# Performance work log

Measured on AMD Instinct MI355X. Metric: run time of the kernel, lower is better.

Reference implementation:

```python
import math
import jax, jax.numpy as jnp
import numpy as np

B, N, CS, CZ, CH, H, PQ, PV = 1, 4096, 512, 128, 64, 16, 4, 8
BQ, BK = 32, 128
NB = N // BQ
CZ4 = CZ // 4
INF = 100000.0
EPS = 1e-8


def quat_to_rot(q):
    w, x, y, z = q[..., 0], q[..., 1], q[..., 2], q[..., 3]
    return jnp.stack([
        jnp.stack([1 - 2 * (y * y + z * z), 2 * (x * y - w * z), 2 * (x * z + w * y)], -1),
        jnp.stack([2 * (x * y + w * z), 1 - 2 * (x * x + z * z), 2 * (y * z - w * x)], -1),
        jnp.stack([2 * (x * z - w * y), 2 * (y * z + w * x), 1 - 2 * (x * x + y * y)], -1),
    ], -2)


def setup_inputs() -> dict:
    key = jax.random.key(0)
    ks = jax.random.split(key, 16)
    s = jax.random.normal(ks[0], (B, N, CS), jnp.float32)
    z = jax.random.normal(ks[1], (B, NB, BQ, BK, CZ), jnp.float32)
    trans = jax.random.normal(ks[2], (B, N, 3), jnp.float32) * 10.0
    quat = jax.random.normal(ks[3], (B, N, 4), jnp.float32)
    quat = quat / jnp.linalg.norm(quat, axis=-1, keepdims=True)
    rots = quat_to_rot(quat)
    s_mask = jnp.ones((B, N), jnp.float32)
    pad = (BK - BQ) // 2  # key window centered on each query block
    key_idx = (jnp.arange(NB)[:, None] * BQ - pad + jnp.arange(BK)[None, :]).astype(jnp.int32)

    def w(k, shp):
        return jax.random.normal(k, shp, jnp.float32) * (1.0 / math.sqrt(shp[0]))

    return {
        's': s, 'z': z, 'trans': trans, 'rots': rots, 's_mask': s_mask, 'key_idx': key_idx,
        'Wq': w(ks[4], (CS, H * CH)), 'Wk': w(ks[5], (CS, H * CH)), 'Wv': w(ks[6], (CS, H * CH)),
        'Wqp': w(ks[7], (CS, H * PQ * 3)), 'Wkvp': w(ks[8], (CS, H * (PQ + PV) * 3)),
        'Wb': w(ks[9], (CZ, H)), 'Wdz': w(ks[10], (CZ, CZ4)),
        'head_weights': jnp.full((H,), float(np.log(np.e - 1.0)), jnp.float32),  # softplus^-1(1)
        'Wout': w(ks[11], (H * (CZ4 + CH + PV * 4), CS)),
        'g_s': jnp.ones((CS,), jnp.float32), 'b_s': jnp.zeros((CS,), jnp.float32),
        'g_z': jnp.ones((CZ,), jnp.float32), 'b_z': jnp.zeros((CZ,), jnp.float32),
    }


def _ln(x, g, b):
    m = jnp.mean(x, -1, keepdims=True)
    v = jnp.mean((x - m) ** 2, -1, keepdims=True)
    return (x - m) * jax.lax.rsqrt(v + 1e-5) * g + b


def _ipa(s, z, trans, rots, s_mask, key_idx, Wq, Wk, Wv, Wqp, Wkvp, Wb, Wdz,
         head_weights, Wout, g_s, b_s, g_z, b_z):
    s_n = _ln(s, g_s, b_s)
    z_n = _ln(z, g_z, b_z)

    valid = (key_idx >= 0) & (key_idx < N)            # [NB, BK]
    idx = jnp.clip(key_idx, 0, N - 1)
    vf = valid.astype(s.dtype)[None]                  # [1, NB, BK]

    def gk(x):  # gather key window: [B,N,...] -> [B,NB,BK,...]
        return x[:, idx]

    sq = s_n.reshape(B, NB, BQ, CS)
    sk = gk(s_n) * vf[..., None]                      # zero-pad out-of-range keys

    tq = trans.reshape(B, NB, BQ, 3)
    rq = rots.reshape(B, NB, BQ, 3, 3)
    tk = gk(trans) * vf[..., None]
    rk = jnp.where(valid[None, :, :, None, None], gk(rots), jnp.eye(3, dtype=rots.dtype))

    q = (sq @ Wq).reshape(B, NB, BQ, H, CH)
    k = (sk @ Wk).reshape(B, NB, BK, H, CH)
    v = (sk @ Wv).reshape(B, NB, BK, H, CH)

    q_pts = (sq @ Wqp).reshape(B, NB, BQ, H * PQ, 3)
    q_pts = jnp.einsum('bnqij,bnqpj->bnqpi', rq, q_pts) + tq[:, :, :, None, :]
    q_pts = q_pts.reshape(B, NB, BQ, H, PQ, 3)

    kv_pts = (sk @ Wkvp).reshape(B, NB, BK, H * (PQ + PV), 3)
    kv_pts = jnp.einsum('bnkij,bnkpj->bnkpi', rk, kv_pts) + tk[:, :, :, None, :]
    kv_pts = kv_pts.reshape(B, NB, BK, H, PQ + PV, 3)
    k_pts, v_pts = kv_pts[..., :PQ, :], kv_pts[..., PQ:, :]

    bias = jnp.einsum('bnqkc,ch->bnqkh', z_n, Wb)
    a = jnp.einsum('bnqhc,bnkhc->bnqkh', q, k) * math.sqrt(1.0 / (3 * CH))
    a = a + math.sqrt(1.0 / 3) * bias

    disp = q_pts[:, :, :, None] - k_pts[:, :, None]   # [B,NB,BQ,BK,H,PQ,3]
    pt_att = jnp.sum(disp ** 2, -1)                   # [B,NB,BQ,BK,H,PQ]
    hw = jax.nn.softplus(head_weights) * math.sqrt(1.0 / (3 * (PQ * 9.0 / 2)))
    pt_att = -0.5 * jnp.sum(pt_att * hw[:, None], -1)  # [B,NB,BQ,BK,H]

    qm = s_mask.reshape(B, NB, BQ)
    km = gk(s_mask) * vf
    amask = INF * (qm[:, :, :, None] * km[:, :, None, :] - 1.0)

    a = a + pt_att + amask[..., None]
    a = jax.nn.softmax(jnp.swapaxes(a, -1, -2), axis=-1)  # [B,NB,BQ,H,BK]

    o = jnp.einsum('bnqhk,bnkhc->bnqhc', a, v).reshape(B, NB, BQ, H * CH)

    o_pt = jnp.einsum('bnqhk,bnkhpc->bnqhpc', a, v_pts)
    o_pt = jnp.einsum('bnqji,bnqhpj->bnqhpi', rq, o_pt - tq[:, :, :, None, None, :])
    o_pt_norm = jnp.sqrt(jnp.sum(o_pt ** 2, -1) + EPS).reshape(B, NB, BQ, H * PV)
    o_pt = o_pt.reshape(B, NB, BQ, H * PV * 3)

    pair_z = z_n @ Wdz                                # [B,NB,BQ,BK,CZ4]
    o_pair = jnp.einsum('bnqhk,bnqkc->bnqhc', a, pair_z).reshape(B, NB, BQ, H * CZ4)

    out = jnp.concatenate([o, o_pt, o_pt_norm, o_pair], -1) @ Wout
    return out.reshape(B, N, CS)


def reference(s, z, trans, rots, s_mask, key_idx, Wq, Wk, Wv, Wqp, Wkvp, Wb, Wdz,
              head_weights, Wout, g_s, b_s, g_z, b_z):
    return _ipa(s, z, trans, rots, s_mask, key_idx, Wq, Wk, Wv, Wqp, Wkvp, Wb, Wdz,
                head_weights, Wout, g_s, b_s, g_z, b_z)
```

## Files before the change

### kernel.cpp

```cpp
#include <hip/hip_runtime.h>
#include <math.h>

#define D_N 4096
#define PBW 3072
#define PPW 768
#define OFFK 1024
#define OFFV 2048
#define CATW 2048

typedef __bf16 bf16_t;
typedef __bf16 bf16x8 __attribute__((ext_vector_type(8)));
typedef __bf16 bf16x4 __attribute__((ext_vector_type(4)));
typedef float f32x4 __attribute__((ext_vector_type(4)));

__device__ __forceinline__ void gld16(const void* g, void* l) {
    __builtin_amdgcn_global_load_lds((const __attribute__((address_space(1))) unsigned int*)g,
                                     (__attribute__((address_space(3))) unsigned int*)l, 16, 0, 0);
}

__global__ __launch_bounds__(256) void k_prep(
    const float* __restrict__ Wq, const float* __restrict__ Wk, const float* __restrict__ Wv,
    const float* __restrict__ Wqp, const float* __restrict__ Wkvp, const float* __restrict__ Wout,
    const float* __restrict__ Wb, const float* __restrict__ Wdz,
    const float* __restrict__ gz, const float* __restrict__ bz,
    const float* __restrict__ s, const float* __restrict__ g_s, const float* __restrict__ b_s,
    bf16_t* __restrict__ wcatT, bf16_t* __restrict__ WoutT,
    bf16_t* __restrict__ WzT, float* __restrict__ Kv, bf16_t* __restrict__ s_nb)
{
    __shared__ float T[64][65];
    const int bx = blockIdx.x;
    const int tid = threadIdx.x;
    if (bx < 736) {
        const float* src; int ld, coff, r0;
        bf16_t* dst; int Rdst;
        if (bx < 480) {
            int c0 = (bx % 60) * 64;
            r0 = (bx / 60) * 64;
            if (c0 < 1024)      { src = Wq;   ld = 1024; coff = c0; }
            else if (c0 < 2048) { src = Wk;   ld = 1024; coff = c0 - 1024; }
            else if (c0 < 3072) { src = Wv;   ld = 1024; coff = c0 - 2048; }
            else if (c0 < 3264) { src = Wqp;  ld = 192;  coff = c0 - 3072; }
            else                { src = Wkvp; ld = 576;  coff = c0 - 3264; }
            dst = wcatT + (size_t)c0 * 512; Rdst = 512;
        } else {
            int b = bx - 480;
            int c0 = (b & 7) * 64;
            r0 = (b >> 3) * 64;
            src = Wout; ld = 512; coff = c0;
            dst = WoutT + (size_t)c0 * 2048; Rdst = 2048;
        }
        {
            int rr = tid >> 2, cb = (tid & 3) * 16;
            const float* p = src + (size_t)(r0 + rr) * ld + coff + cb;
            #pragma unroll
            for (int i = 0; i < 4; ++i)
                *(float4*)&T[rr][cb + i * 4] = *(const float4*)(p + i * 4);
        }
        __syncthreads();
        {
            int cc = tid >> 2, rb = (tid & 3) * 16;
            bf16_t* o = dst + (size_t)cc * Rdst + r0 + rb;
            bf16x8 o0, o1;
            #pragma unroll
            for (int j = 0; j < 8; ++j) o0[j] = (bf16_t)T[rb + j][cc];
            #pragma unroll
            for (int j = 0; j < 8; ++j) o1[j] = (bf16_t)T[rb + 8 + j][cc];
            *(bf16x8*)(o) = o0;
            *(bf16x8*)(o + 8) = o1;
        }
    } else if (bx == 736) {
        for (int i = tid; i < 6144; i += 256) {
            int j = i >> 7, c = i & 127;
            float w = (j < 16) ? Wb[c * 16 + j] : Wdz[c * 32 + (j - 16)];
            WzT[i] = (bf16_t)(gz[c] * w);
        }
        if (tid < 48) {
            int j = tid;
            float acc = 0.f;
            for (int c = 0; c < 128; ++c) {
                float w = (j < 16) ? Wb[c * 16 + j] : Wdz[c * 32 + (j - 16)];
                acc += bz[c] * w;
            }
            Kv[j] = acc;
        }
    } else {
        int row = (bx - 737) * 4 + (tid >> 6);
        int lane = tid & 63;
        const float4* p = (const float4*)(s + (size_t)row * 512);
        float4 v0 = p[lane];
        float4 v1 = p[lane + 64];
        float sum = v0.x + v0.y + v0.z + v0.w + v1.x + v1.y + v1.z + v1.w;
        float sq  = v0.x*v0.x + v0.y*v0.y + v0.z*v0.z + v0.w*v0.w
                  + v1.x*v1.x + v1.y*v1.y + v1.z*v1.z + v1.w*v1.w;
        #pragma unroll
        for (int off = 1; off < 64; off <<= 1) {
            sum += __shfl_xor(sum, off);
            sq  += __shfl_xor(sq, off);
        }
        float m = sum * (1.0f / 512.0f);
        float var = sq * (1.0f / 512.0f) - m * m;
        float rs = rsqrtf(var + 1e-5f);
        int c = lane * 4;
        int c2 = 256 + lane * 4;
        bf16x4 r0, r1;
        r0[0] = (bf16_t)((v0.x - m) * rs * g_s[c+0] + b_s[c+0]);
        r0[1] = (bf16_t)((v0.y - m) * rs * g_s[c+1] + b_s[c+1]);
        r0[2] = (bf16_t)((v0.z - m) * rs * g_s[c+2] + b_s[c+2]);
        r0[3] = (bf16_t)((v0.w - m) * rs * g_s[c+3] + b_s[c+3]);
        r1[0] = (bf16_t)((v1.x - m) * rs * g_s[c2+0] + b_s[c2+0]);
        r1[1] = (bf16_t)((v1.y - m) * rs * g_s[c2+1] + b_s[c2+1]);
        r1[2] = (bf16_t)((v1.z - m) * rs * g_s[c2+2] + b_s[c2+2]);
        r1[3] = (bf16_t)((v1.w - m) * rs * g_s[c2+3] + b_s[c2+3]);
        *(bf16x4*)(s_nb + (size_t)row * 512 + c)  = r0;
        *(bf16x4*)(s_nb + (size_t)row * 512 + c2) = r1;
    }
}

__global__ __launch_bounds__(256) void k_fused(
    const bf16_t* __restrict__ A, const bf16_t* __restrict__ BT,
    bf16_t* __restrict__ projb, float* __restrict__ projp,
    const float* __restrict__ z, const bf16_t* __restrict__ WzT, const float* __restrict__ Kv,
    bf16_t* __restrict__ biasT, bf16_t* __restrict__ pzT)
{
    __shared__ bf16_t Asl[128][32];
    __shared__ bf16_t Bsl[128][32];
    const int bx = blockIdx.x;
    const int tid = threadIdx.x, lane = tid & 63, w = tid >> 6;
    int gemm_id = -1, zid = 0;
    if (bx < 2880) {
        int s3 = bx % 3, b3 = bx / 3;
        if (s3 == 0) gemm_id = b3;
        else         zid = b3 * 2 + s3 - 1;
    } else {
        zid = 1920 + (bx - 2880);
    }

    if (gemm_id >= 0) {
        const int row0 = (gemm_id / 30) * 128, col0 = (gemm_id % 30) * 128;
        const int wr = (w >> 1) * 64, wc = (w & 1) * 64;
        const int K = 512;
        const int sr = lane >> 2, k8 = (lane & 3) * 8;
        const bf16_t* Ab = A + (size_t)(row0 + w * 32 + sr) * K + k8;
        const bf16_t* Bb = BT + (size_t)(col0 + w * 32 + sr) * K + k8;
        f32x4 acc[4][4];
        #pragma unroll
        for (int m = 0; m < 4; ++m)
            #pragma unroll
            for (int n = 0; n < 4; ++n) acc[m][n] = (f32x4){0.f,0.f,0.f,0.f};
        for (int k0 = 0; k0 < K; k0 += 32) {
            __syncthreads();
            gld16(Ab + k0,          &Asl[w * 32][0]);
            gld16(Ab + k0 + 16 * K, &Asl[w * 32 + 16][0]);
            gld16(Bb + k0,          &Bsl[w * 32][0]);
            gld16(Bb + k0 + 16 * K, &Bsl[w * 32 + 16][0]);
            __syncthreads();
            bf16x8 af[4], bfr[4];
            #pragma unroll
            for (int m = 0; m < 4; ++m) af[m]  = *(const bf16x8*)&Asl[wr + m*16 + (lane & 15)][(lane >> 4) * 8];
            #pragma unroll
            for (int n = 0; n < 4; ++n) bfr[n] = *(const bf16x8*)&Bsl[wc + n*16 + (lane & 15)][(lane >> 4) * 8];
            #pragma unroll
            for (int m = 0; m < 4; ++m)
                #pragma unroll
                for (int n = 0; n < 4; ++n)
                    acc[m][n] = __builtin_amdgcn_mfma_f32_16x16x32_bf16(af[m], bfr[n], acc[m][n], 0, 0, 0);
        }
        if (col0 < 3072) {
            #pragma unroll
            for (int m = 0; m < 4; ++m)
                #pragma unroll
                for (int n = 0; n < 4; ++n)
                    #pragma unroll
                    for (int i = 0; i < 4; ++i)
                        projb[(size_t)(row0 + wr + m*16 + (lane >> 4)*4 + i) * PBW + col0 + wc + n*16 + (lane & 15)]
                            = (bf16_t)acc[m][n][i];
        } else {
            #pragma unroll
            for (int m = 0; m < 4; ++m)
                #pragma unroll
                for (int n = 0; n < 4; ++n)
                    #pragma unroll
                    for (int i = 0; i < 4; ++i)
                        projp[(size_t)(row0 + wr + m*16 + (lane >> 4)*4 + i) * PPW + col0 - 3072 + wc + n*16 + (lane & 15)]
                            = acc[m][n][i];
        }
        return;
    }

    const int r16 = lane & 15, kg = lane >> 4;
    bf16x8 bfz[3][4];
    #pragma unroll
    for (int nt = 0; nt < 3; ++nt)
        #pragma unroll
        for (int kc = 0; kc < 4; ++kc)
            bfz[nt][kc] = *(const bf16x8*)(WzT + (size_t)(nt * 16 + r16) * 128 + kc * 32 + kg * 8);
    const float K0 = Kv[r16], K1 = Kv[16 + r16], K2 = Kv[32 + r16];
    const int gid = zid * 4 + w;

    #pragma unroll 2
    for (int it = 0; it < 4; ++it) {
        const int t_ = gid * 4 + it;
        const float* zp = z + ((size_t)t_ * 16 + r16) * 128 + kg * 8;
        float4 za[4], zc[4];
        float sum = 0.f, sq = 0.f;
        #pragma unroll
        for (int kc = 0; kc < 4; ++kc) {
            za[kc] = *(const float4*)(zp + kc * 32);
            zc[kc] = *(const float4*)(zp + kc * 32 + 4);
            sum += za[kc].x + za[kc].y + za[kc].z + za[kc].w + zc[kc].x + zc[kc].y + zc[kc].z + zc[kc].w;
            sq  += za[kc].x*za[kc].x + za[kc].y*za[kc].y + za[kc].z*za[kc].z + za[kc].w*za[kc].w
                 + zc[kc].x*zc[kc].x + zc[kc].y*zc[kc].y + zc[kc].z*zc[kc].z + zc[kc].w*zc[kc].w;
        }
        sum += __shfl_xor(sum, 16); sq += __shfl_xor(sq, 16);
        sum += __shfl_xor(sum, 32); sq += __shfl_xor(sq, 32);
        float m_ = sum * (1.0f / 128.0f);
        float rs_ = rsqrtf(sq * (1.0f / 128.0f) - m_ * m_ + 1e-5f);
        bf16x8 af[4];
        #pragma unroll
        for (int kc = 0; kc < 4; ++kc) {
            af[kc][0] = (bf16_t)((za[kc].x - m_) * rs_);
            af[kc][1] = (bf16_t)((za[kc].y - m_) * rs_);
            af[kc][2] = (bf16_t)((za[kc].z - m_) * rs_);
            af[kc][3] = (bf16_t)((za[kc].w - m_) * rs_);
            af[kc][4] = (bf16_t)((zc[kc].x - m_) * rs_);
            af[kc][5] = (bf16_t)((zc[kc].y - m_) * rs_);
            af[kc][6] = (bf16_t)((zc[kc].z - m_) * rs_);
            af[kc][7] = (bf16_t)((zc[kc].w - m_) * rs_);
        }
        f32x4 acc0 = (f32x4){0.f,0.f,0.f,0.f};
        f32x4 acc1 = (f32x4){0.f,0.f,0.f,0.f};
        f32x4 acc2 = (f32x4){0.f,0.f,0.f,0.f};
        #pragma unroll
        for (int kc = 0; kc < 4; ++kc) {
            acc0 = __builtin_amdgcn_mfma_f32_16x16x32_bf16(af[kc], bfz[0][kc], acc0, 0, 0, 0);
            acc1 = __builtin_amdgcn_mfma_f32_16x16x32_bf16(af[kc], bfz[1][kc], acc1, 0, 0, 0);
            acc2 = __builtin_amdgcn_mfma_f32_16x16x32_bf16(af[kc], bfz[2][kc], acc2, 0, 0, 0);
        }
        const int rowq_ = t_ >> 3;
        const int k0_ = ((t_ & 7) << 4) + kg * 4;
        bf16x4 bb, p1, p2;
        #pragma unroll
        for (int i2 = 0; i2 < 4; ++i2) {
            bb[i2] = (bf16_t)(acc0[i2] + K0);
            p1[i2] = (bf16_t)(acc1[i2] + K1);
            p2[i2] = (bf16_t)(acc2[i2] + K2);
        }
        *(bf16x4*)&biasT[((size_t)rowq_ * 16 + r16) * 128 + k0_] = bb;
        *(bf16x4*)&pzT[((size_t)rowq_ * 32 + r16) * 128 + k0_] = p1;
        *(bf16x4*)&pzT[((size_t)rowq_ * 32 + 16 + r16) * 128 + k0_] = p2;
    }
}

__global__ __launch_bounds__(256, 3) void k_attn4(
    const bf16_t* __restrict__ projb, const float* __restrict__ projp,
    const bf16_t* __restrict__ biasT, const float* __restrict__ rots,
    const float* __restrict__ trans, const float* __restrict__ smask,
    const int* __restrict__ kidx, const float* __restrict__ hwraw,
    bf16_t* __restrict__ catb, bf16_t* __restrict__ Pbf)
{
    __shared__ __align__(16) char pool[51840];
    bf16_t (*Qs)[72]   = (bf16_t(*)[72])pool;
    bf16_t (*Ks)[72]   = (bf16_t(*)[72])(pool + 32 * 72 * 2);
    bf16_t (*Vt)[136]  = (bf16_t(*)[136])pool;
    float  (*att)[132] = (float(*)[132])(pool + 26112);
    bf16_t (*Ps)[136]  = (bf16_t(*)[136])(pool + 26112);
    float  (*optmp)[33]= (float(*)[33])(pool + 26112 + 8704);
    float  (*kp_s)[12] = (float(*)[12])(pool + 43008);
    float  (*qp_s)[12] = (float(*)[12])(pool + 49152);
    float*  km_s       = (float*)(pool + 50688);
    float*  qm_s       = (float*)(pool + 51200);

    const int wgid = blockIdx.x;
    const int swz = (wgid & 7) * 256 + (wgid >> 3);
    const int h = swz >> 7;
    const int nblk = swz & 127;
    const int tid = threadIdx.x;
    const int lane = tid & 63;
    const int w = tid >> 6;
    const int rowq0 = nblk * 32;
    const float hw = log1pf(__expf(hwraw[h])) * 0.13608276348795434f;

    const int kslot = tid & 127;
    const int ki = kidx[nblk * 128 + kslot];
    const int kvalid = (ki >= 0 && ki < D_N);
    const int myrow = ki < 0 ? 0 : (ki > D_N - 1 ? D_N - 1 : ki);

    {
        int q = tid >> 3, cg = (tid & 7) * 8;
        *(bf16x8*)&Qs[q][cg] = *(const bf16x8*)(projb + (size_t)(rowq0 + q) * PBW + h * 64 + cg);
    }
    float Rk[9], tk0 = 0.f, tk1 = 0.f, tk2 = 0.f;
    bf16x8 vreg[8];
    if (tid < 128) {
        km_s[tid] = kvalid ? smask[myrow] : 0.0f;
        const float* Rp = rots + (size_t)myrow * 9;
        const float* tp = trans + (size_t)myrow * 3;
        #pragma unroll
        for (int e = 0; e < 9; ++e) Rk[e] = Rp[e];
        tk0 = tp[0]; tk1 = tp[1]; tk2 = tp[2];
        const float* kp = projp + (size_t)myrow * PPW + 192 + h * 36;
        float4 p0 = *(const float4*)kp;
        float4 p1 = *(const float4*)(kp + 4);
        float4 p2 = *(const float4*)(kp + 8);
        float xs[4] = {p0.x, p0.w, p1.z, p2.y};
        float ys[4] = {p0.y, p1.x, p1.w, p2.z};
        float zs[4] = {p0.z, p1.y, p2.x, p2.w};
        #pragma unroll
        for (int p = 0; p < 4; ++p) {
            kp_s[tid][p*3+0] = Rk[0]*xs[p] + Rk[1]*ys[p] + Rk[2]*zs[p] + tk0;
            kp_s[tid][p*3+1] = Rk[3]*xs[p] + Rk[4]*ys[p] + Rk[5]*zs[p] + tk1;
            kp_s[tid][p*3+2] = Rk[6]*xs[p] + Rk[7]*ys[p] + Rk[8]*zs[p] + tk2;
        }
    } else {
        if (tid < 160) qm_s[tid - 128] = smask[rowq0 + tid - 128];
        int j = tid - 128;
        {
            int q = j >> 2, p = j & 3;
            const float* Rp = rots + (size_t)(rowq0 + q) * 9;
            const float* tp = trans + (size_t)(rowq0 + q) * 3;
            const float* qp = projp + (size_t)(rowq0 + q) * PPW + h * 12 + p * 3;
            float x = qp[0], y = qp[1], zc = qp[2];
            qp_s[q][p*3+0] = Rp[0]*x + Rp[1]*y + Rp[2]*zc + tp[0];
            qp_s[q][p*3+1] = Rp[3]*x + Rp[4]*y + Rp[5]*zc + tp[1];
            qp_s[q][p*3+2] = Rp[6]*x + Rp[7]*y + Rp[8]*zc + tp[2];
        }
        {
            const bf16_t* pK = projb + (size_t)myrow * PBW + OFFK + h * 64;
            #pragma unroll
            for (int u = 0; u < 8; ++u)
                *(bf16x8*)&Ks[j][u * 8] = *(const bf16x8*)(pK + u * 8);
        }
        {
            const bf16_t* pV = projb + (size_t)myrow * PBW + OFFV + h * 64;
            #pragma unroll
            for (int u4 = 0; u4 < 8; ++u4)
                vreg[u4] = *(const bf16x8*)(pV + u4 * 8);
        }
    }
    float bT_reg[16];
    {
        int q = tid >> 3, kg = tid & 7;
        const bf16_t* bT = biasT + ((size_t)(rowq0 + q) * 16 + h) * 128 + kg;
        #pragma unroll
        for (int j2 = 0; j2 < 16; ++j2) bT_reg[j2] = (float)bT[j2 * 8];
    }
    __syncthreads();
    {
        #pragma unroll
        for (int j = 0; j < 4; ++j) {
            int T = w * 4 + j;
            int m = T & 1, n = T >> 1;
            f32x4 acc = (f32x4){0.f,0.f,0.f,0.f};
            #pragma unroll
            for (int kc = 0; kc < 2; ++kc) {
                bf16x8 a = *(const bf16x8*)&Qs[m*16 + (lane & 15)][kc*32 + (lane >> 4) * 8];
                bf16x8 b = *(const bf16x8*)&Ks[n*16 + (lane & 15)][kc*32 + (lane >> 4) * 8];
                acc = __builtin_amdgcn_mfma_f32_16x16x32_bf16(a, b, acc, 0, 0, 0);
            }
            #pragma unroll
            for (int i = 0; i < 4; ++i)
                att[m*16 + (lane >> 4)*4 + i][n*16 + (lane & 15)] = acc[i];
        }
    }
    __syncthreads();
    if (tid < 128) {
        const float* vp = projp + (size_t)myrow * PPW + 192 + h * 36 + 12;
        float4 a0 = *(const float4*)(vp);
        float4 a1 = *(const float4*)(vp + 4);
        float4 a2 = *(const float4*)(vp + 8);
        float4 a3 = *(const float4*)(vp + 12);
        float4 a4 = *(const float4*)(vp + 16);
        float4 a5 = *(const float4*)(vp + 20);
        float xs[8] = {a0.x, a0.w, a1.z, a2.y, a3.x, a3.w, a4.z, a5.y};
        float ys[8] = {a0.y, a1.x, a1.w, a2.z, a3.y, a4.x, a4.w, a5.z};
        float zs[8] = {a0.z, a1.y, a2.x, a2.w, a3.z, a4.y, a5.x, a5.w};
        #pragma unroll
        for (int p = 0; p < 8; ++p) {
            Vt[64 + p*3 + 0][tid] = (bf16_t)(Rk[0]*xs[p] + Rk[1]*ys[p] + Rk[2]*zs[p] + tk0);
            Vt[64 + p*3 + 1][tid] = (bf16_t)(Rk[3]*xs[p] + Rk[4]*ys[p] + Rk[5]*zs[p] + tk1);
            Vt[64 + p*3 + 2][tid] = (bf16_t)(Rk[6]*xs[p] + Rk[7]*ys[p] + Rk[8]*zs[p] + tk2);
        }
        {
            bf16x8 zz = {};
            *(bf16x8*)&Vt[88 + (tid & 7)][(tid >> 3) * 8] = zz;
        }
    } else {
        int krow = tid - 128;
        #pragma unroll
        for (int u4 = 0; u4 < 8; ++u4) {
            #pragma unroll
            for (int jj = 0; jj < 8; ++jj) Vt[u4 * 8 + jj][krow] = vreg[u4][jj];
        }
    }
    {
        int q = tid >> 3, kg = tid & 7;
        float qp[12];
        #pragma unroll
        for (int e = 0; e < 12; ++e) qp[e] = qp_s[q][e];
        float qm = qm_s[q];
        #pragma unroll
        for (int j2 = 0; j2 < 16; ++j2) {
            int k = kg + j2 * 8;
            float4 k0 = *(const float4*)&kp_s[k][0];
            float4 k1 = *(const float4*)&kp_s[k][4];
            float4 k2 = *(const float4*)&kp_s[k][8];
            float d0 = qp[0]-k0.x, d1 = qp[1]-k0.y, d2_ = qp[2]-k0.z, d3 = qp[3]-k0.w;
            float d4 = qp[4]-k1.x, d5 = qp[5]-k1.y, d6 = qp[6]-k1.z, d7 = qp[7]-k1.w;
            float d8 = qp[8]-k2.x, d9 = qp[9]-k2.y, d10 = qp[10]-k2.z, d11 = qp[11]-k2.w;
            float dd = d0*d0+d1*d1+d2_*d2_+d3*d3+d4*d4+d5*d5+d6*d6+d7*d7+d8*d8+d9*d9+d10*d10+d11*d11;
            float val = att[q][k] * 0.07216878364870323f
                      + 0.5773502691896258f * bT_reg[j2]
                      + 100000.0f * (qm * km_s[k] - 1.0f)
                      - 0.5f * hw * dd;
            att[q][k] = val;
        }
    }
    __syncthreads();
    {
        int q = tid >> 3, kg = tid & 7;
        float l[16];
        #pragma unroll
        for (int j2 = 0; j2 < 16; ++j2) l[j2] = att[q][kg * 16 + j2];
        float mx = l[0];
        #pragma unroll
        for (int j2 = 1; j2 < 16; ++j2) mx = fmaxf(mx, l[j2]);
        mx = fmaxf(mx, __shfl_xor(mx, 1));
        mx = fmaxf(mx, __shfl_xor(mx, 2));
        mx = fmaxf(mx, __shfl_xor(mx, 4));
        float se = 0.f;
        #pragma unroll
        for (int j2 = 0; j2 < 16; ++j2) { l[j2] = __expf(l[j2] - mx); se += l[j2]; }
        se += __shfl_xor(se, 1);
        se += __shfl_xor(se, 2);
        se += __shfl_xor(se, 4);
        float inv = 1.0f / se;
        __syncthreads();
        bf16_t* pg = Pbf + ((size_t)(rowq0 + q) * 16 + h) * 128 + kg * 16;
        #pragma unroll
        for (int j4 = 0; j4 < 4; ++j4) {
            bf16x4 pb4;
            #pragma unroll
            for (int e = 0; e < 4; ++e) pb4[e] = (bf16_t)(l[j4 * 4 + e] * inv);
            *(bf16x4*)&Ps[q][kg * 16 + j4 * 4] = pb4;
            *(bf16x4*)(pg + j4 * 4) = pb4;
        }
    }
    __syncthreads();
    {
        #pragma unroll
        for (int j = 0; j < 3; ++j) {
            int T = w * 3 + j;
            int m = T & 1, n = T >> 1;
            f32x4 acc = (f32x4){0.f,0.f,0.f,0.f};
            #pragma unroll
            for (int kc = 0; kc < 4; ++kc) {
                bf16x8 a = *(const bf16x8*)&Ps[m*16 + (lane & 15)][kc*32 + (lane >> 4) * 8];
                bf16x8 b = *(const bf16x8*)&Vt[n*16 + (lane & 15)][kc*32 + (lane >> 4) * 8];
                acc = __builtin_amdgcn_mfma_f32_16x16x32_bf16(a, b, acc, 0, 0, 0);
            }
            int rowb = m * 16 + (lane >> 4) * 4;
            int col = lane & 15;
            if (n < 4) {
                #pragma unroll
                for (int i = 0; i < 4; ++i)
                    catb[(size_t)(rowq0 + rowb + i) * CATW + h * 64 + n * 16 + col] = (bf16_t)acc[i];
            } else {
                #pragma unroll
                for (int i = 0; i < 4; ++i)
                    optmp[rowb + i][(n - 4) * 16 + col] = acc[i];
            }
        }
    }
    __syncthreads();
    {
        int q = tid >> 3, pp = tid & 7;
        float sx = optmp[q][pp * 3 + 0];
        float sy = optmp[q][pp * 3 + 1];
        float sz = optmp[q][pp * 3 + 2];
        const float* R = rots + (size_t)(rowq0 + q) * 9;
        const float* t = trans + (size_t)(rowq0 + q) * 3;
        float x = sx - t[0], y = sy - t[1], z2 = sz - t[2];
        float ox = R[0] * x + R[3] * y + R[6] * z2;
        float oy = R[1] * x + R[4] * y + R[7] * z2;
        float oz = R[2] * x + R[5] * y + R[8] * z2;
        bf16_t* cp = catb + (size_t)(rowq0 + q) * CATW;
        cp[1024 + h * 24 + pp * 3 + 0] = (bf16_t)ox;
        cp[1024 + h * 24 + pp * 3 + 1] = (bf16_t)oy;
        cp[1024 + h * 24 + pp * 3 + 2] = (bf16_t)oz;
        cp[1408 + h * 8 + pp] = (bf16_t)sqrtf(ox * ox + oy * oy + oz * oz + 1e-8f);
    }
}

__global__ __launch_bounds__(256) void k_opair(const bf16_t* __restrict__ Pbf,
    const bf16_t* __restrict__ pzT, bf16_t* __restrict__ catb)
{
    int tid = threadIdx.x, lane = tid & 63, w = tid >> 6;
    size_t rowq = (size_t)blockIdx.x * 4 + w;
    const bf16_t* Pp = Pbf + rowq * 2048;
    const bf16_t* zp = pzT + rowq * 4096;
    bf16x8 pa[4];
    #pragma unroll
    for (int kc = 0; kc < 4; ++kc)
        pa[kc] = *(const bf16x8*)(Pp + (size_t)(lane & 15) * 128 + kc * 32 + (lane >> 4) * 8);
    #pragma unroll
    for (int ct = 0; ct < 2; ++ct) {
        f32x4 acc = (f32x4){0.f,0.f,0.f,0.f};
        #pragma unroll
        for (int kc = 0; kc < 4; ++kc) {
            bf16x8 b = *(const bf16x8*)(zp + (size_t)(ct * 16 + (lane & 15)) * 128 + kc * 32 + (lane >> 4) * 8);
            acc = __builtin_amdgcn_mfma_f32_16x16x32_bf16(pa[kc], b, acc, 0, 0, 0);
        }
        #pragma unroll
        for (int i = 0; i < 4; ++i) {
            int hh = (lane >> 4) * 4 + i;
            catb[rowq * CATW + 1536 + hh * 32 + ct * 16 + (lane & 15)] = (bf16_t)acc[i];
        }
    }
}

__global__ __launch_bounds__(256) void gemm_out(const bf16_t* __restrict__ A, const bf16_t* __restrict__ BT,
    float* __restrict__ C)
{
    __shared__ bf16_t Asl[64][32];
    __shared__ bf16_t Bsl[128][32];
    const int tid = threadIdx.x, lane = tid & 63, w = tid >> 6;
    const int by = blockIdx.x & 63, bxc = blockIdx.x >> 6;
    const int row0 = by * 64, col0 = bxc * 128;
    const int wr = (w >> 1) * 32, wc = (w & 1) * 64;
    const int K = 2048;
    const int sr = lane >> 2, k8 = (lane & 3) * 8;
    const bf16_t* Ab = A + (size_t)(row0 + w * 16 + sr) * K + k8;
    const bf16_t* Bb = BT + (size_t)(col0 + w * 32 + sr) * K + k8;
    f32x4 acc[2][4];
    #pragma unroll
    for (int m = 0; m < 2; ++m)
        #pragma unroll
        for (int n = 0; n < 4; ++n) acc[m][n] = (f32x4){0.f,0.f,0.f,0.f};
    for (int k0 = 0; k0 < K; k0 += 32) {
        __syncthreads();
        gld16(Ab + k0,          &Asl[w * 16][0]);
        gld16(Bb + k0,          &Bsl[w * 32][0]);
        gld16(Bb + k0 + 16 * K, &Bsl[w * 32 + 16][0]);
        __syncthreads();
        bf16x8 af[2], bfr[4];
        #pragma unroll
        for (int m = 0; m < 2; ++m) af[m]  = *(const bf16x8*)&Asl[wr + m*16 + (lane & 15)][(lane >> 4) * 8];
        #pragma unroll
        for (int n = 0; n < 4; ++n) bfr[n] = *(const bf16x8*)&Bsl[wc + n*16 + (lane & 15)][(lane >> 4) * 8];
        #pragma unroll
        for (int m = 0; m < 2; ++m)
            #pragma unroll
            for (int n = 0; n < 4; ++n)
                acc[m][n] = __builtin_amdgcn_mfma_f32_16x16x32_bf16(af[m], bfr[n], acc[m][n], 0, 0, 0);
    }
    #pragma unroll
    for (int m = 0; m < 2; ++m)
        #pragma unroll
        for (int n = 0; n < 4; ++n)
            #pragma unroll
            for (int i = 0; i < 4; ++i)
                C[(size_t)(row0 + wr + m*16 + (lane >> 4)*4 + i) * 512 + col0 + wc + n*16 + (lane & 15)] = acc[m][n][i];
}

extern "C" void kernel_launch(void* const* d_in, const int* in_sizes, int n_in,
                              void* d_out, int out_size, void* d_ws, size_t ws_size,
                              hipStream_t stream)
{
    (void)in_sizes; (void)n_in; (void)out_size;
    const float* s     = (const float*)d_in[0];
    const float* z     = (const float*)d_in[1];
    const float* trans = (const float*)d_in[2];
    const float* rots  = (const float*)d_in[3];
    const float* smask = (const float*)d_in[4];
    const int*   kidx  = (const int*)d_in[5];
    const float* Wq    = (const float*)d_in[6];
    const float* Wk    = (const float*)d_in[7];
    const float* Wv    = (const float*)d_in[8];
    const float* Wqp   = (const float*)d_in[9];
    const float* Wkvp  = (const float*)d_in[10];
    const float* Wb    = (const float*)d_in[11];
    const float* Wdz   = (const float*)d_in[12];
    const float* hw    = (const float*)d_in[13];
    const float* Wout  = (const float*)d_in[14];
    const float* g_s   = (const float*)d_in[15];
    const float* b_s   = (const float*)d_in[16];
    const float* g_z   = (const float*)d_in[17];
    const float* b_z   = (const float*)d_in[18];

    char* ws = (char*)d_ws;
    bf16_t* projb = (bf16_t*)(ws);
    float*  projp = (float*)(ws + 25165824);
    bf16_t* biasT = (bf16_t*)(ws + 37748736);
    bf16_t* wcatT = (bf16_t*)(ws + 71303168);
    bf16_t* s_nb  = (bf16_t*)(ws + 75235328);
    bf16_t* pzT   = (bf16_t*)(ws + 79429632);
    bf16_t* Pbf   = (bf16_t*)(ws + 112984064);
    bf16_t* catb  = (bf16_t*)(ws + 129761280);
    bf16_t* WoutT = (bf16_t*)(ws + 146538496);
    bf16_t* WzT   = (bf16_t*)(ws + 148635648);
    float*  Kv    = (float*)(ws + 148647936);
    if (ws_size < (size_t)148648128) return;
    float* out = (float*)d_out;

    k_prep<<<1761, 256, 0, stream>>>(Wq, Wk, Wv, Wqp, Wkvp, Wout, Wb, Wdz, g_z, b_z,
                                     s, g_s, b_s, wcatT, WoutT, WzT, Kv, s_nb);
    k_fused<<<3008, 256, 0, stream>>>(s_nb, wcatT, projb, projp, z, WzT, Kv, biasT, pzT);
    k_attn4<<<2048, 256, 0, stream>>>(projb, projp, biasT, rots, trans, smask, kidx, hw, catb, Pbf);
    k_opair<<<1024, 256, 0, stream>>>(Pbf, pzT, catb);
    gemm_out<<<256, 256, 0, stream>>>(catb, WoutT, out);
}
```

Measured before the change: 202.3 us.

## Fuse pair-output contraction into attention kernel and reswizzle block-to-XCD mapping

The separate k_opair kernel is removed. The attention-weighted pair-feature contraction now runs inside the attention kernel, reading the softmax probabilities straight from shared memory instead of writing them to a global Pbf buffer and reading them back. This saves a launch plus a write and read of the probability tensor, but pzT is read once per head block (16 times per query row) and the contraction runs as scalar FMAs instead of MFMA. The block index swizzle is also changed so that all heads of a query block land on the same XCD, to improve L2 reuse of pzT and projb.

Result: slower. 297.8 us (+47.2%).

```diff
diff --git a/kernel.cpp b/kernel.cpp
--- a/kernel.cpp
+++ b/kernel.cpp
@@ -251,12 +251,12 @@
     }
 }
 
-__global__ __launch_bounds__(256, 3) void k_attn4(
+__global__ __launch_bounds__(256, 3) void k_attn5(
     const bf16_t* __restrict__ projb, const float* __restrict__ projp,
     const bf16_t* __restrict__ biasT, const float* __restrict__ rots,
     const float* __restrict__ trans, const float* __restrict__ smask,
     const int* __restrict__ kidx, const float* __restrict__ hwraw,
-    bf16_t* __restrict__ catb, bf16_t* __restrict__ Pbf)
+    const bf16_t* __restrict__ pzT, bf16_t* __restrict__ catb)
 {
     __shared__ __align__(16) char pool[51840];
     bf16_t (*Qs)[72]   = (bf16_t(*)[72])pool;
@@ -271,9 +271,11 @@
     float*  qm_s       = (float*)(pool + 51200);
 
     const int wgid = blockIdx.x;
-    const int swz = (wgid & 7) * 256 + (wgid >> 3);
-    const int h = swz >> 7;
-    const int nblk = swz & 127;
+    const int xcd = wgid & 7;
+    const int lo2 = (wgid >> 3) & 3;
+    const int h   = (wgid >> 5) & 15;
+    const int hi  = wgid >> 9;
+    const int nblk = (hi << 5) | (xcd << 2) | lo2;
     const int tid = threadIdx.x;
     const int lane = tid & 63;
     const int w = tid >> 6;
@@ -435,14 +437,12 @@
         se += __shfl_xor(se, 4);
         float inv = 1.0f / se;
         __syncthreads();
-        bf16_t* pg = Pbf + ((size_t)(rowq0 + q) * 16 + h) * 128 + kg * 16;
         #pragma unroll
         for (int j4 = 0; j4 < 4; ++j4) {
             bf16x4 pb4;
             #pragma unroll
             for (int e = 0; e < 4; ++e) pb4[e] = (bf16_t)(l[j4 * 4 + e] * inv);
             *(bf16x4*)&Ps[q][kg * 16 + j4 * 4] = pb4;
-            *(bf16x4*)(pg + j4 * 4) = pb4;
         }
     }
     __syncthreads();
@@ -489,32 +489,27 @@
         cp[1024 + h * 24 + pp * 3 + 2] = (bf16_t)oz;
         cp[1408 + h * 8 + pp] = (bf16_t)sqrtf(ox * ox + oy * oy + oz * oz + 1e-8f);
     }
-}
-
-__global__ __launch_bounds__(256) void k_opair(const bf16_t* __restrict__ Pbf,
-    const bf16_t* __restrict__ pzT, bf16_t* __restrict__ catb)
-{
-    int tid = threadIdx.x, lane = tid & 63, w = tid >> 6;
-    size_t rowq = (size_t)blockIdx.x * 4 + w;
-    const bf16_t* Pp = Pbf + rowq * 2048;
-    const bf16_t* zp = pzT + rowq * 4096;
-    bf16x8 pa[4];
-    #pragma unroll
-    for (int kc = 0; kc < 4; ++kc)
-        pa[kc] = *(const bf16x8*)(Pp + (size_t)(lane & 15) * 128 + kc * 32 + (lane >> 4) * 8);
-    #pragma unroll
-    for (int ct = 0; ct < 2; ++ct) {
-        f32x4 acc = (f32x4){0.f,0.f,0.f,0.f};
-        #pragma unroll
-        for (int kc = 0; kc < 4; ++kc) {
-            bf16x8 b = *(const bf16x8*)(zp + (size_t)(ct * 16 + (lane & 15)) * 128 + kc * 32 + (lane >> 4) * 8);
-            acc = __builtin_amdgcn_mfma_f32_16x16x32_bf16(pa[kc], b, acc, 0, 0, 0);
-        }
-        #pragma unroll
-        for (int i = 0; i < 4; ++i) {
-            int hh = (lane >> 4) * 4 + i;
-            catb[rowq * CATW + 1536 + hh * 32 + ct * 16 + (lane & 15)] = (bf16_t)acc[i];
-        }
+    {
+        int q = tid >> 3, cg = (tid & 7) * 4;
+        const bf16_t* pzrow = pzT + ((size_t)(rowq0 + q) * 32 + cg) * 128;
+        float acc[4] = {0.f, 0.f, 0.f, 0.f};
+        #pragma unroll
+        for (int kc = 0; kc < 16; ++kc) {
+            bf16x8 ps8 = *(const bf16x8*)&Ps[q][kc * 8];
+            float psf[8];
+            #pragma unroll
+            for (int e = 0; e < 8; ++e) psf[e] = (float)ps8[e];
+            #pragma unroll
+            for (int c = 0; c < 4; ++c) {
+                bf16x8 pz8 = *(const bf16x8*)(pzrow + (size_t)c * 128 + kc * 8);
+                #pragma unroll
+                for (int e = 0; e < 8; ++e) acc[c] += psf[e] * (float)pz8[e];
+            }
+        }
+        bf16x4 ov;
+        #pragma unroll
+        for (int c = 0; c < 4; ++c) ov[c] = (bf16_t)acc[c];
+        *(bf16x4*)&catb[(size_t)(rowq0 + q) * CATW + 1536 + h * 32 + cg] = ov;
     }
 }
 
@@ -594,7 +589,6 @@
     bf16_t* wcatT = (bf16_t*)(ws + 71303168);
     bf16_t* s_nb  = (bf16_t*)(ws + 75235328);
     bf16_t* pzT   = (bf16_t*)(ws + 79429632);
-    bf16_t* Pbf   = (bf16_t*)(ws + 112984064);
     bf16_t* catb  = (bf16_t*)(ws + 129761280);
     bf16_t* WoutT = (bf16_t*)(ws + 146538496);
     bf16_t* WzT   = (bf16_t*)(ws + 148635648);
@@ -605,7 +599,6 @@
     k_prep<<<1761, 256, 0, stream>>>(Wq, Wk, Wv, Wqp, Wkvp, Wout, Wb, Wdz, g_z, b_z,
                                      s, g_s, b_s, wcatT, WoutT, WzT, Kv, s_nb);
     k_fused<<<3008, 256, 0, stream>>>(s_nb, wcatT, projb, projp, z, WzT, Kv, biasT, pzT);
-    k_attn4<<<2048, 256, 0, stream>>>(projb, projp, biasT, rots, trans, smask, kidx, hw, catb, Pbf);
-    k_opair<<<1024, 256, 0, stream>>>(Pbf, pzT, catb);
+    k_attn5<<<2048, 256, 0, stream>>>(projb, projp, biasT, rots, trans, smask, kidx, hw, pzT, catb);
     gemm_out<<<256, 256, 0, stream>>>(catb, WoutT, out);
 }
```

## Overlap opair kernel with first K-slice of output GEMM via split-K

Applied to the files above, without the earlier changes.

Splits the output projection GEMM along K: columns 0..1535 of catb (already written by attention) are multiplied inside the same launch as the o_pair kernel, using extra blocks. A second kernel then handles the remaining 512 K columns that depend on o_pair and accumulates into the output. This lets the o_pair work and most of the GEMM run concurrently and shortens the dependent tail, at the cost of an extra read-modify-write of the fp32 output.

After: 205.6 us. Within noise of the previous version (+1.7%).

```diff
diff --git a/kernel.cpp b/kernel.cpp
--- a/kernel.cpp
+++ b/kernel.cpp
@@ -491,34 +491,77 @@
     }
 }
 
-__global__ __launch_bounds__(256) void k_opair(const bf16_t* __restrict__ Pbf,
-    const bf16_t* __restrict__ pzT, bf16_t* __restrict__ catb)
+__global__ __launch_bounds__(256) void k_opair_gemm1(const bf16_t* __restrict__ Pbf,
+    const bf16_t* __restrict__ pzT, bf16_t* __restrict__ catb,
+    const bf16_t* __restrict__ WoutT, float* __restrict__ C)
 {
-    int tid = threadIdx.x, lane = tid & 63, w = tid >> 6;
-    size_t rowq = (size_t)blockIdx.x * 4 + w;
-    const bf16_t* Pp = Pbf + rowq * 2048;
-    const bf16_t* zp = pzT + rowq * 4096;
-    bf16x8 pa[4];
+    __shared__ bf16_t Asl[64][32];
+    __shared__ bf16_t Bsl[128][32];
+    const int tid = threadIdx.x, lane = tid & 63, w = tid >> 6;
+    if (blockIdx.x < 1024) {
+        size_t rowq = (size_t)blockIdx.x * 4 + w;
+        const bf16_t* Pp = Pbf + rowq * 2048;
+        const bf16_t* zp = pzT + rowq * 4096;
+        bf16x8 pa[4];
+        #pragma unroll
+        for (int kc = 0; kc < 4; ++kc)
+            pa[kc] = *(const bf16x8*)(Pp + (size_t)(lane & 15) * 128 + kc * 32 + (lane >> 4) * 8);
+        #pragma unroll
+        for (int ct = 0; ct < 2; ++ct) {
+            f32x4 acc = (f32x4){0.f,0.f,0.f,0.f};
+            #pragma unroll
+            for (int kc = 0; kc < 4; ++kc) {
+                bf16x8 b = *(const bf16x8*)(zp + (size_t)(ct * 16 + (lane & 15)) * 128 + kc * 32 + (lane >> 4) * 8);
+                acc = __builtin_amdgcn_mfma_f32_16x16x32_bf16(pa[kc], b, acc, 0, 0, 0);
+            }
+            #pragma unroll
+            for (int i = 0; i < 4; ++i) {
+                int hh = (lane >> 4) * 4 + i;
+                catb[rowq * CATW + 1536 + hh * 32 + ct * 16 + (lane & 15)] = (bf16_t)acc[i];
+            }
+        }
+        return;
+    }
+    const int id = blockIdx.x - 1024;
+    const int by = id & 63, bxc = id >> 6;
+    const int row0 = by * 64, col0 = bxc * 128;
+    const int wr = (w >> 1) * 32, wc = (w & 1) * 64;
+    const int K = 2048;
+    const int sr = lane >> 2, k8 = (lane & 3) * 8;
+    const bf16_t* Ab = catb + (size_t)(row0 + w * 16 + sr) * K + k8;
+    const bf16_t* Bb = WoutT + (size_t)(col0 + w * 32 + sr) * K + k8;
+    f32x4 acc[2][4];
     #pragma unroll
-    for (int kc = 0; kc < 4; ++kc)
-        pa[kc] = *(const bf16x8*)(Pp + (size_t)(lane & 15) * 128 + kc * 32 + (lane >> 4) * 8);
+    for (int m = 0; m < 2; ++m)
+        #pragma unroll
+        for (int n = 0; n < 4; ++n) acc[m][n] = (f32x4){0.f,0.f,0.f,0.f};
+    for (int k0 = 0; k0 < 1536; k0 += 32) {
+        __syncthreads();
+        gld16(Ab + k0,          &Asl[w * 16][0]);
+        gld16(Bb + k0,          &Bsl[w * 32][0]);
+        gld16(Bb + k0 + 16 * K, &Bsl[w * 32 + 16][0]);
+        __syncthreads();
+        bf16x8 af[2], bfr[4];
+        #pragma unroll
+        for (int m = 0; m < 2; ++m) af[m]  = *(const bf16x8*)&Asl[wr + m*16 + (lane & 15)][(lane >> 4) * 8];
+        #pragma unroll
+        for (int n = 0; n < 4; ++n) bfr[n] = *(const bf16x8*)&Bsl[wc + n*16 + (lane & 15)][(lane >> 4) * 8];
+        #pragma unroll
+        for (int m = 0; m < 2; ++m)
+            #pragma unroll
+            for (int n = 0; n < 4; ++n)
+                acc[m][n] = __builtin_amdgcn_mfma_f32_16x16x32_bf16(af[m], bfr[n], acc[m][n], 0, 0, 0);
+    }
     #pragma unroll
-    for (int ct = 0; ct < 2; ++ct) {
-        f32x4 acc = (f32x4){0.f,0.f,0.f,0.f};
-        #pragma unroll
-        for (int kc = 0; kc < 4; ++kc) {
-            bf16x8 b = *(const bf16x8*)(zp + (size_t)(ct * 16 + (lane & 15)) * 128 + kc * 32 + (lane >> 4) * 8);
-            acc = __builtin_amdgcn_mfma_f32_16x16x32_bf16(pa[kc], b, acc, 0, 0, 0);
-        }
-        #pragma unroll
-        for (int i = 0; i < 4; ++i) {
-            int hh = (lane >> 4) * 4 + i;
-            catb[rowq * CATW + 1536 + hh * 32 + ct * 16 + (lane & 15)] = (bf16_t)acc[i];
-        }
-    }
+    for (int m = 0; m < 2; ++m)
+        #pragma unroll
+        for (int n = 0; n < 4; ++n)
+            #pragma unroll
+            for (int i = 0; i < 4; ++i)
+                C[(size_t)(row0 + wr + m*16 + (lane >> 4)*4 + i) * 512 + col0 + wc + n*16 + (lane & 15)] = acc[m][n][i];
 }
 
-__global__ __launch_bounds__(256) void gemm_out(const bf16_t* __restrict__ A, const bf16_t* __restrict__ BT,
+__global__ __launch_bounds__(256) void k_gemm2(const bf16_t* __restrict__ A, const bf16_t* __restrict__ BT,
     float* __restrict__ C)
 {
     __shared__ bf16_t Asl[64][32];
@@ -536,7 +579,7 @@
     for (int m = 0; m < 2; ++m)
         #pragma unroll
         for (int n = 0; n < 4; ++n) acc[m][n] = (f32x4){0.f,0.f,0.f,0.f};
-    for (int k0 = 0; k0 < K; k0 += 32) {
+    for (int k0 = 1536; k0 < 2048; k0 += 32) {
         __syncthreads();
         gld16(Ab + k0,          &Asl[w * 16][0]);
         gld16(Bb + k0,          &Bsl[w * 32][0]);
@@ -558,8 +601,10 @@
         #pragma unroll
         for (int n = 0; n < 4; ++n)
             #pragma unroll
-            for (int i = 0; i < 4; ++i)
-                C[(size_t)(row0 + wr + m*16 + (lane >> 4)*4 + i) * 512 + col0 + wc + n*16 + (lane & 15)] = acc[m][n][i];
+            for (int i = 0; i < 4; ++i) {
+                size_t idx = (size_t)(row0 + wr + m*16 + (lane >> 4)*4 + i) * 512 + col0 + wc + n*16 + (lane & 15);
+                C[idx] = C[idx] + acc[m][n][i];
+            }
 }
 
 extern "C" void kernel_launch(void* const* d_in, const int* in_sizes, int n_in,
@@ -606,6 +651,6 @@
                                      s, g_s, b_s, wcatT, WoutT, WzT, Kv, s_nb);
     k_fused<<<3008, 256, 0, stream>>>(s_nb, wcatT, projb, projp, z, WzT, Kv, biasT, pzT);
     k_attn4<<<2048, 256, 0, stream>>>(projb, projp, biasT, rots, trans, smask, kidx, hw, catb, Pbf);
-    k_opair<<<1024, 256, 0, stream>>>(Pbf, pzT, catb);
-    gemm_out<<<256, 256, 0, stream>>>(catb, WoutT, out);
+    k_opair_gemm1<<<1280, 256, 0, stream>>>(Pbf, pzT, catb, WoutT, out);
+    k_gemm2<<<256, 256, 0, stream>>>(catb, WoutT, out);
 }
```
